# Performance work log

Measured on AMD Instinct MI355X. Metric: run time of the kernel, lower is better.

## Reference

```python
import jax, jax.numpy as jnp
import numpy as np

DIM = 1024
N_HEADS = 16
HEAD_DIM = DIM // N_HEADS  # 64
THETA = 10000.0
B, S = 4, 1024


def _rope_full_dim(x):
    """RoPE applied over the FULL last dim (head_dim == model dim), matching the
    original module which builds RotaryEmbeddings(head_dim=args.dim) and applies
    it to [B, S, dim] before splitting into heads. Positions start at 0."""
    Bx, Sx, D = x.shape
    freq = 1.0 / (THETA ** (jnp.arange(0, D, 2, dtype=jnp.float32) / D))  # [D/2]
    ang = jnp.arange(Sx, dtype=jnp.float32)[:, None] * freq[None, :]      # [S, D/2]
    cos, sin = jnp.cos(ang), jnp.sin(ang)
    xp = x.astype(jnp.float32).reshape(Bx, Sx, D // 2, 2)
    x0, x1 = xp[..., 0], xp[..., 1]
    rot = jnp.stack([x0 * cos - x1 * sin, x0 * sin + x1 * cos], axis=-1)
    return rot.reshape(Bx, Sx, D).astype(x.dtype)


def setup_inputs() -> dict:
    key = jax.random.key(0)
    ks = jax.random.split(key, 5)
    scale = 1.0 / np.sqrt(DIM)
    x = jax.random.normal(ks[0], (B, S, DIM), dtype=jnp.float32)
    Wq = jax.random.normal(ks[1], (DIM, DIM), dtype=jnp.float32) * scale
    Wk = jax.random.normal(ks[2], (DIM, DIM), dtype=jnp.float32) * scale
    Wv = jax.random.normal(ks[3], (DIM, DIM), dtype=jnp.float32) * scale
    Wo = jax.random.normal(ks[4], (DIM, DIM), dtype=jnp.float32) * scale
    bo = jnp.zeros((DIM,), dtype=jnp.float32)
    return {"x": x, "Wq": Wq, "Wk": Wk, "Wv": Wv, "Wo": Wo, "bo": bo, "start_pos": 0}


def reference(x, Wq, Wk, Wv, Wo, bo, start_pos):
    # start_pos == 0: the zero-initialized KV cache write+read is an identity
    # (keys == xk, values == xv over [:, :S]); n_rep == 1 so repeat_kv is a no-op.
    # NOTE: the original applies NO causal mask.
    Bx, Sx, _ = x.shape
    xq = _rope_full_dim(x @ Wq.T)  # [B, S, DIM] (weights stored torch-style [out,in])
    xk = _rope_full_dim(x @ Wk.T)
    xv = x @ Wv.T
    q = xq.reshape(Bx, Sx, N_HEADS, HEAD_DIM).transpose(0, 2, 1, 3)  # [B,H,S,D]
    k = xk.reshape(Bx, Sx, N_HEADS, HEAD_DIM).transpose(0, 2, 1, 3)
    v = xv.reshape(Bx, Sx, N_HEADS, HEAD_DIM).transpose(0, 2, 1, 3)
    scores = jnp.einsum("bhqd,bhkd->bhqk", q, k) / np.float32(np.sqrt(HEAD_DIM))
    attn = jax.nn.softmax(scores.astype(jnp.float32), axis=-1).astype(q.dtype)
    out = jnp.einsum("bhqk,bhkd->bhqd", attn, v)          # [B,H,S,D]
    out = out.transpose(0, 2, 1, 3).reshape(Bx, Sx, DIM)  # [B,S,DIM]
    return out @ Wo.T + bo
```

## Files before the change

### kernel.cpp

```cpp
#include <hip/hip_runtime.h>
#include <cstdint>
#include <cstddef>

typedef _Float16 f16;
typedef __attribute__((ext_vector_type(8))) _Float16 h8v;
typedef __attribute__((ext_vector_type(4))) _Float16 h4v;
typedef __attribute__((ext_vector_type(4))) float f4v;

#define DIM 1024
#define SEQ 1024
#define NH 16
#define HD 64

__device__ __forceinline__ void gld16(const void* g, void* l) {
  __builtin_amdgcn_global_load_lds(
      (const __attribute__((address_space(1))) void*)g,
      (__attribute__((address_space(3))) void*)l, 16, 0, 0);
}

__device__ __forceinline__ f4v mfma16(h8v a, h8v b, f4v c) {
  return __builtin_amdgcn_mfma_f32_16x16x32_f16(a, b, c, 0, 0, 0);
}

__device__ __forceinline__ void cvt_store4(f16* dst, float4 v) {
  *(h4v*)dst = (h4v){(f16)v.x, (f16)v.y, (f16)v.z, (f16)v.w};
}

__global__ __launch_bounds__(256) void convert_kernel(
    const float* __restrict__ x,  const float* __restrict__ Wq,
    const float* __restrict__ Wk, const float* __restrict__ Wv,
    const float* __restrict__ Wo,
    f16* __restrict__ xh, f16* __restrict__ wqkv, f16* __restrict__ woh)
{
  int i = blockIdx.x * 256 + threadIdx.x;
  cvt_store4(xh + 4 * (size_t)i, ((const float4*)x)[i]);
  if (i < DIM * DIM / 4) {
    cvt_store4(wqkv + 4 * (size_t)i,               ((const float4*)Wq)[i]);
    cvt_store4(wqkv + DIM * DIM + 4 * (size_t)i,   ((const float4*)Wk)[i]);
    cvt_store4(wqkv + 2 * DIM * DIM + 4 * (size_t)i, ((const float4*)Wv)[i]);
    cvt_store4(woh + 4 * (size_t)i,                ((const float4*)Wo)[i]);
  }
}

__global__ __launch_bounds__(256) void qkv_gemm(
    const f16* __restrict__ A, const f16* __restrict__ W,
    f16* __restrict__ Qh, f16* __restrict__ Kh, f16* __restrict__ Vt)
{
  __shared__ f16 lA[128 * 32];
  __shared__ f16 lB[128 * 32];
  const int m0 = blockIdx.x * 128;
  const int n0 = blockIdx.y * 128;
  const int tid = threadIdx.x;
  const int w = tid >> 6, lane = tid & 63, quad = lane >> 4, l16 = lane & 15;
  const int wm = (w >> 1) * 64, wn = (w & 1) * 64;

  const int c0 = tid, c1 = 256 + tid;
  const int r0 = c0 >> 2, kc0 = (c0 & 3) ^ ((r0 >> 1) & 3);
  const int r1 = c1 >> 2, kc1 = (c1 & 3) ^ ((r1 >> 1) & 3);
  const f16* gA0 = A + (size_t)(m0 + r0) * DIM + kc0 * 8;
  const f16* gA1 = A + (size_t)(m0 + r1) * DIM + kc1 * 8;
  const f16* gB0 = W + (size_t)(n0 + r0) * DIM + kc0 * 8;
  const f16* gB1 = W + (size_t)(n0 + r1) * DIM + kc1 * 8;
  f16* lA0 = &lA[(c0 & ~63) * 8];
  f16* lA1 = &lA[(c1 & ~63) * 8];
  f16* lB0 = &lB[(c0 & ~63) * 8];
  f16* lB1 = &lB[(c1 & ~63) * 8];

  int pA[4], pB[4];
#pragma unroll
  for (int t = 0; t < 4; ++t) {
    int r = wm + t * 16 + l16;
    pA[t] = r * 4 + (quad ^ ((r >> 1) & 3));
    int rn = wn + t * 16 + l16;
    pB[t] = rn * 4 + (quad ^ ((rn >> 1) & 3));
  }

  f4v acc[4][4] = {};
  for (int kt = 0; kt < DIM / 32; ++kt) {
    const int ko = kt * 32;
    gld16(gA0 + ko, lA0);
    gld16(gA1 + ko, lA1);
    gld16(gB0 + ko, lB0);
    gld16(gB1 + ko, lB1);
    __syncthreads();
    h8v af[4], bf[4];
#pragma unroll
    for (int t = 0; t < 4; ++t) af[t] = *(const h8v*)&lA[pA[t] * 8];
#pragma unroll
    for (int t = 0; t < 4; ++t) bf[t] = *(const h8v*)&lB[pB[t] * 8];
#pragma unroll
    for (int i = 0; i < 4; ++i)
#pragma unroll
      for (int j = 0; j < 4; ++j)
        acc[i][j] = mfma16(af[i], bf[j], acc[i][j]);
    __syncthreads();
  }

  if (n0 < 2 * DIM) {
    f16* dst = (n0 < DIM) ? Qh : Kh;
#pragma unroll
    for (int i = 0; i < 4; ++i) {
      const int mb = m0 + wm + i * 16 + quad * 4;
#pragma unroll
      for (int j = 0; j < 4; ++j) {
        const int n = n0 + wn + j * 16 + l16;
        const int d = n & (DIM - 1);
        const float fr = exp2f(-0.025952563f * (float)(d >> 1));
        const float sgn = (d & 1) ? 1.0f : -1.0f;
        const int hh = d >> 6, dd = d & 63;
#pragma unroll
        for (int r = 0; r < 4; ++r) {
          const int m = mb + r;
          const int s = m & (SEQ - 1), b = m >> 10;
          const float v = acc[i][j][r];
          const float pt = __shfl_xor(v, 1, 64);
          float sn, cs;
          __sincosf((float)s * fr, &sn, &cs);
          dst[((size_t)(b * NH + hh) * SEQ + s) * HD + dd] =
              (f16)(v * cs + sgn * pt * sn);
        }
      }
    }
  } else {
#pragma unroll
    for (int i = 0; i < 4; ++i) {
      const int mb = m0 + wm + i * 16 + quad * 4;
      const int s = mb & (SEQ - 1), b = mb >> 10;
#pragma unroll
      for (int j = 0; j < 4; ++j) {
        const int d = (n0 - 2 * DIM) + wn + j * 16 + l16;
        const int hh = d >> 6, dd = d & 63;
        h4v vv = {(f16)acc[i][j][0], (f16)acc[i][j][1],
                  (f16)acc[i][j][2], (f16)acc[i][j][3]};
        *(h4v*)&Vt[((size_t)(b * NH + hh) * HD + dd) * SEQ + s] = vv;
      }
    }
  }
}

__global__ __launch_bounds__(256) void attn_kernel(
    const f16* __restrict__ Q, const f16* __restrict__ K,
    const f16* __restrict__ V, f16* __restrict__ O)
{
  __shared__ f16 lK[64 * 64];
  __shared__ f16 lV[64 * 64];
  __shared__ f16 lP[4][16 * 72];
  const int tid = threadIdx.x;
  const int w = tid >> 6, lane = tid & 63, quad = lane >> 4, l16 = lane & 15;
  const int qt = blockIdx.x, bh = blockIdx.y;
  const f16* Qb = Q + (size_t)bh * SEQ * HD;
  const f16* Kb = K + (size_t)bh * SEQ * HD;
  const f16* Vb = V + (size_t)bh * HD * SEQ;
  const int q0 = qt * 64;
  const int qrow = q0 + w * 16 + l16;

  h8v aq0 = *(const h8v*)&Qb[(size_t)qrow * HD + quad * 8];
  h8v aq1 = *(const h8v*)&Qb[(size_t)qrow * HD + quad * 8 + 32];
  aq0 = aq0 * (f16)0.125f;
  aq1 = aq1 * (f16)0.125f;

  const int c0 = tid, c1 = 256 + tid;
  const int r0 = c0 >> 3, kc0 = (c0 & 7) ^ (r0 & 7);
  const int r1 = c1 >> 3, kc1 = (c1 & 7) ^ (r1 & 7);
  const f16* gK0 = Kb + (size_t)r0 * HD + kc0 * 8;
  const f16* gK1 = Kb + (size_t)r1 * HD + kc1 * 8;
  const f16* gV0 = Vb + (size_t)r0 * SEQ + kc0 * 8;
  const f16* gV1 = Vb + (size_t)r1 * SEQ + kc1 * 8;
  f16* lK0 = &lK[(c0 & ~63) * 8];
  f16* lK1 = &lK[(c1 & ~63) * 8];
  f16* lV0 = &lV[(c0 & ~63) * 8];
  f16* lV1 = &lV[(c1 & ~63) * 8];

  int pbt[4][2];
#pragma unroll
  for (int j = 0; j < 4; ++j) {
    int r = j * 16 + l16;
#pragma unroll
    for (int kk = 0; kk < 2; ++kk)
      pbt[j][kk] = r * 8 + ((quad + 4 * kk) ^ (r & 7));
  }

  float mr[4], lr[4];
  f4v accO[4] = {};
#pragma unroll
  for (int r = 0; r < 4; ++r) { mr[r] = -1e30f; lr[r] = 0.f; }

  for (int t = 0; t < SEQ / 64; ++t) {
    const int key0 = t * 64;
    __syncthreads();
    gld16(gK0 + (size_t)key0 * HD, lK0);
    gld16(gK1 + (size_t)key0 * HD, lK1);
    gld16(gV0 + key0, lV0);
    gld16(gV1 + key0, lV1);
    __syncthreads();

    f4v sc[4];
#pragma unroll
    for (int j = 0; j < 4; ++j) {
      f4v z = {};
      z = mfma16(aq0, *(const h8v*)&lK[pbt[j][0] * 8], z);
      z = mfma16(aq1, *(const h8v*)&lK[pbt[j][1] * 8], z);
      sc[j] = z;
    }
    float tmax[4];
#pragma unroll
    for (int r = 0; r < 4; ++r) {
      float tm = fmaxf(fmaxf(sc[0][r], sc[1][r]), fmaxf(sc[2][r], sc[3][r]));
#pragma unroll
      for (int off = 1; off < 16; off <<= 1)
        tm = fmaxf(tm, __shfl_xor(tm, off, 64));
      tmax[r] = tm;
    }
    float alpha[4], mnew[4];
#pragma unroll
    for (int r = 0; r < 4; ++r) {
      mnew[r] = fmaxf(mr[r], tmax[r]);
      alpha[r] = __expf(mr[r] - mnew[r]);
      mr[r] = mnew[r];
    }
    float p[4][4];
    float rs[4] = {0.f, 0.f, 0.f, 0.f};
#pragma unroll
    for (int j = 0; j < 4; ++j)
#pragma unroll
      for (int r = 0; r < 4; ++r) {
        p[j][r] = __expf(sc[j][r] - mnew[r]);
        rs[r] += p[j][r];
      }
#pragma unroll
    for (int r = 0; r < 4; ++r) {
#pragma unroll
      for (int off = 1; off < 16; off <<= 1)
        rs[r] += __shfl_xor(rs[r], off, 64);
      lr[r] = lr[r] * alpha[r] + rs[r];
    }
    f4v av = {alpha[0], alpha[1], alpha[2], alpha[3]};
#pragma unroll
    for (int j = 0; j < 4; ++j) accO[j] *= av;

    f16* Pw = lP[w];
#pragma unroll
    for (int j = 0; j < 4; ++j)
#pragma unroll
      for (int r = 0; r < 4; ++r)
        Pw[(quad * 4 + r) * 72 + j * 16 + l16] = (f16)p[j][r];
    h8v pa0 = *(const h8v*)&Pw[l16 * 72 + quad * 8];
    h8v pa1 = *(const h8v*)&Pw[l16 * 72 + quad * 8 + 32];
#pragma unroll
    for (int j = 0; j < 4; ++j) {
      accO[j] = mfma16(pa0, *(const h8v*)&lV[pbt[j][0] * 8], accO[j]);
      accO[j] = mfma16(pa1, *(const h8v*)&lV[pbt[j][1] * 8], accO[j]);
    }
  }

  const int b = bh >> 4, hh = bh & 15;
  f4v inv = {1.f / lr[0], 1.f / lr[1], 1.f / lr[2], 1.f / lr[3]};
#pragma unroll
  for (int j = 0; j < 4; ++j) {
    f4v o = accO[j] * inv;
    const int d = j * 16 + l16;
#pragma unroll
    for (int r = 0; r < 4; ++r) {
      const int s = q0 + w * 16 + quad * 4 + r;
      O[(size_t)(b * SEQ + s) * DIM + hh * HD + d] = (f16)o[r];
    }
  }
}

__global__ __launch_bounds__(256) void out_gemm(
    const f16* __restrict__ A, const f16* __restrict__ W,
    const float* __restrict__ bias, float* __restrict__ out)
{
  __shared__ f16 lA[64 * 32];
  __shared__ f16 lB[128 * 32];
  const int m0 = blockIdx.x * 64;
  const int n0 = blockIdx.y * 128;
  const int tid = threadIdx.x;
  const int w = tid >> 6, lane = tid & 63, quad = lane >> 4, l16 = lane & 15;
  const int wm = (w >> 1) * 32, wn = (w & 1) * 64;

  const int c0 = tid, c1 = 256 + tid;
  const int rA = c0 >> 2, kcA = (c0 & 3) ^ ((rA >> 1) & 3);
  const int rB1 = c1 >> 2, kcB1 = (c1 & 3) ^ ((rB1 >> 1) & 3);
  const f16* gA  = A + (size_t)(m0 + rA) * DIM + kcA * 8;
  const f16* gB0 = W + (size_t)(n0 + rA) * DIM + kcA * 8;
  const f16* gB1 = W + (size_t)(n0 + rB1) * DIM + kcB1 * 8;
  f16* lAp  = &lA[(c0 & ~63) * 8];
  f16* lB0p = &lB[(c0 & ~63) * 8];
  f16* lB1p = &lB[(c1 & ~63) * 8];

  int pA_[2], pB_[4];
#pragma unroll
  for (int t = 0; t < 2; ++t) {
    int r = wm + t * 16 + l16;
    pA_[t] = r * 4 + (quad ^ ((r >> 1) & 3));
  }
#pragma unroll
  for (int t = 0; t < 4; ++t) {
    int rn = wn + t * 16 + l16;
    pB_[t] = rn * 4 + (quad ^ ((rn >> 1) & 3));
  }

  f4v acc[2][4] = {};
  for (int kt = 0; kt < DIM / 32; ++kt) {
    const int ko = kt * 32;
    gld16(gA + ko, lAp);
    gld16(gB0 + ko, lB0p);
    gld16(gB1 + ko, lB1p);
    __syncthreads();
    h8v af[2], bf[4];
#pragma unroll
    for (int t = 0; t < 2; ++t) af[t] = *(const h8v*)&lA[pA_[t] * 8];
#pragma unroll
    for (int t = 0; t < 4; ++t) bf[t] = *(const h8v*)&lB[pB_[t] * 8];
#pragma unroll
    for (int i = 0; i < 2; ++i)
#pragma unroll
      for (int j = 0; j < 4; ++j)
        acc[i][j] = mfma16(af[i], bf[j], acc[i][j]);
    __syncthreads();
  }

#pragma unroll
  for (int i = 0; i < 2; ++i) {
#pragma unroll
    for (int j = 0; j < 4; ++j) {
      const int n = n0 + wn + j * 16 + l16;
      const float bv = bias[n];
#pragma unroll
      for (int r = 0; r < 4; ++r) {
        const int m = m0 + wm + i * 16 + quad * 4 + r;
        out[(size_t)m * DIM + n] = acc[i][j][r] + bv;
      }
    }
  }
}

extern "C" void kernel_launch(void* const* d_in, const int* in_sizes, int n_in,
                              void* d_out, int out_size, void* d_ws, size_t ws_size,
                              hipStream_t stream)
{
  (void)in_sizes; (void)n_in; (void)out_size; (void)ws_size;
  const float* x  = (const float*)d_in[0];
  const float* Wq = (const float*)d_in[1];
  const float* Wk = (const float*)d_in[2];
  const float* Wv = (const float*)d_in[3];
  const float* Wo = (const float*)d_in[4];
  const float* bo = (const float*)d_in[5];
  float* out = (float*)d_out;

  char* ws = (char*)d_ws;
  const size_t MB = (size_t)1 << 20;
  f16* xh   = (f16*)(ws);
  f16* wqkv = (f16*)(ws + 8  * MB);
  f16* woh  = (f16*)(ws + 14 * MB);
  f16* Qh   = (f16*)(ws + 16 * MB);
  f16* Kh   = (f16*)(ws + 24 * MB);
  f16* Vt   = (f16*)(ws + 32 * MB);
  f16* Oh   = (f16*)(ws);

  convert_kernel<<<dim3(4096), 256, 0, stream>>>(x, Wq, Wk, Wv, Wo, xh, wqkv, woh);
  qkv_gemm<<<dim3(32, 24), 256, 0, stream>>>(xh, wqkv, Qh, Kh, Vt);
  attn_kernel<<<dim3(16, 64), 256, 0, stream>>>(Qh, Kh, Vt, Oh);
  out_gemm<<<dim3(64, 8), 256, 0, stream>>>(Oh, woh, bo, out);
}
```

Measured before the change: 194.8 us.

## Compute transposed S^T in attention to keep P in registers, drop LDS staging

The QK^T MFMA now takes K as the A operand and Q as B, so each lane holds scores for a single query column across keys. That makes the row max and row sum reductions two cross-quad shuffles instead of four-step butterflies per row. The score accumulator layout then serves directly as the A operand of 16x16x16 MFMAs for P*V, which removes the per-wave LDS write/read round trip for P. In exchange, alpha and the final 1/l must be redistributed with shuffles, and P*V uses twice as many smaller-K MFMAs with new V-tile addressing.

```diff
diff --git a/kernel.cpp b/kernel.cpp
--- a/kernel.cpp
+++ b/kernel.cpp
@@ -20,6 +20,9 @@
 
 __device__ __forceinline__ f4v mfma16(h8v a, h8v b, f4v c) {
   return __builtin_amdgcn_mfma_f32_16x16x32_f16(a, b, c, 0, 0, 0);
+}
+__device__ __forceinline__ f4v mfma16k16(h4v a, h4v b, f4v c) {
+  return __builtin_amdgcn_mfma_f32_16x16x16f16(a, b, c, 0, 0, 0);
 }
 
 __device__ __forceinline__ void cvt_store4(f16* dst, float4 v) {
@@ -144,7 +147,6 @@
 {
   __shared__ f16 lK[64 * 64];
   __shared__ f16 lV[64 * 64];
-  __shared__ f16 lP[4][16 * 72];
   const int tid = threadIdx.x;
   const int w = tid >> 6, lane = tid & 63, quad = lane >> 4, l16 = lane & 15;
   const int qt = blockIdx.x, bh = blockIdx.y;
@@ -154,10 +156,10 @@
   const int q0 = qt * 64;
   const int qrow = q0 + w * 16 + l16;
 
-  h8v aq0 = *(const h8v*)&Qb[(size_t)qrow * HD + quad * 8];
-  h8v aq1 = *(const h8v*)&Qb[(size_t)qrow * HD + quad * 8 + 32];
-  aq0 = aq0 * (f16)0.125f;
-  aq1 = aq1 * (f16)0.125f;
+  h8v bq0 = *(const h8v*)&Qb[(size_t)qrow * HD + quad * 8];
+  h8v bq1 = *(const h8v*)&Qb[(size_t)qrow * HD + quad * 8 + 32];
+  bq0 = bq0 * (f16)0.125f;
+  bq1 = bq1 * (f16)0.125f;
 
   const int c0 = tid, c1 = 256 + tid;
   const int r0 = c0 >> 3, kc0 = (c0 & 7) ^ (r0 & 7);
@@ -179,11 +181,15 @@
     for (int kk = 0; kk < 2; ++kk)
       pbt[j][kk] = r * 8 + ((quad + 4 * kk) ^ (r & 7));
   }
-
-  float mr[4], lr[4];
+  const f16* vbase[4];
+#pragma unroll
+  for (int j = 0; j < 4; ++j) {
+    int slot = (j * 2 + (quad >> 1)) ^ (l16 & 7);
+    vbase[j] = &lV[l16 * 64 + slot * 8 + (quad & 1) * 4];
+  }
+
+  float mr = -1e30f, lr = 0.f;
   f4v accO[4] = {};
-#pragma unroll
-  for (int r = 0; r < 4; ++r) { mr[r] = -1e30f; lr[r] = 0.f; }
 
   for (int t = 0; t < SEQ / 64; ++t) {
     const int key0 = t * 64;
@@ -198,71 +204,66 @@
 #pragma unroll
     for (int j = 0; j < 4; ++j) {
       f4v z = {};
-      z = mfma16(aq0, *(const h8v*)&lK[pbt[j][0] * 8], z);
-      z = mfma16(aq1, *(const h8v*)&lK[pbt[j][1] * 8], z);
+      z = mfma16(*(const h8v*)&lK[pbt[j][0] * 8], bq0, z);
+      z = mfma16(*(const h8v*)&lK[pbt[j][1] * 8], bq1, z);
       sc[j] = z;
     }
-    float tmax[4];
-#pragma unroll
-    for (int r = 0; r < 4; ++r) {
-      float tm = fmaxf(fmaxf(sc[0][r], sc[1][r]), fmaxf(sc[2][r], sc[3][r]));
-#pragma unroll
-      for (int off = 1; off < 16; off <<= 1)
-        tm = fmaxf(tm, __shfl_xor(tm, off, 64));
-      tmax[r] = tm;
-    }
-    float alpha[4], mnew[4];
-#pragma unroll
-    for (int r = 0; r < 4; ++r) {
-      mnew[r] = fmaxf(mr[r], tmax[r]);
-      alpha[r] = __expf(mr[r] - mnew[r]);
-      mr[r] = mnew[r];
-    }
+
+    float tm = sc[0][0];
+#pragma unroll
+    for (int j = 0; j < 4; ++j)
+#pragma unroll
+      for (int r = 0; r < 4; ++r) tm = fmaxf(tm, sc[j][r]);
+    tm = fmaxf(tm, __shfl_xor(tm, 16, 64));
+    tm = fmaxf(tm, __shfl_xor(tm, 32, 64));
+    const float mnew = fmaxf(mr, tm);
+    const float alpha = __expf(mr - mnew);
+    mr = mnew;
+
     float p[4][4];
-    float rs[4] = {0.f, 0.f, 0.f, 0.f};
+    float rs = 0.f;
 #pragma unroll
     for (int j = 0; j < 4; ++j)
 #pragma unroll
       for (int r = 0; r < 4; ++r) {
-        p[j][r] = __expf(sc[j][r] - mnew[r]);
-        rs[r] += p[j][r];
+        p[j][r] = __expf(sc[j][r] - mnew);
+        rs += p[j][r];
       }
-#pragma unroll
-    for (int r = 0; r < 4; ++r) {
-#pragma unroll
-      for (int off = 1; off < 16; off <<= 1)
-        rs[r] += __shfl_xor(rs[r], off, 64);
-      lr[r] = lr[r] * alpha[r] + rs[r];
-    }
-    f4v av = {alpha[0], alpha[1], alpha[2], alpha[3]};
-#pragma unroll
-    for (int j = 0; j < 4; ++j) accO[j] *= av;
-
-    f16* Pw = lP[w];
+    rs += __shfl_xor(rs, 16, 64);
+    rs += __shfl_xor(rs, 32, 64);
+    lr = lr * alpha + rs;
+
+    f4v av;
+#pragma unroll
+    for (int r = 0; r < 4; ++r) av[r] = __shfl(alpha, quad * 4 + r, 64);
+#pragma unroll
+    for (int dt = 0; dt < 4; ++dt) accO[dt] *= av;
+
+    h4v pf[4];
 #pragma unroll
     for (int j = 0; j < 4; ++j)
-#pragma unroll
-      for (int r = 0; r < 4; ++r)
-        Pw[(quad * 4 + r) * 72 + j * 16 + l16] = (f16)p[j][r];
-    h8v pa0 = *(const h8v*)&Pw[l16 * 72 + quad * 8];
-    h8v pa1 = *(const h8v*)&Pw[l16 * 72 + quad * 8 + 32];
-#pragma unroll
-    for (int j = 0; j < 4; ++j) {
-      accO[j] = mfma16(pa0, *(const h8v*)&lV[pbt[j][0] * 8], accO[j]);
-      accO[j] = mfma16(pa1, *(const h8v*)&lV[pbt[j][1] * 8], accO[j]);
-    }
-  }
+      pf[j] = (h4v){(f16)p[j][0], (f16)p[j][1], (f16)p[j][2], (f16)p[j][3]};
+
+#pragma unroll
+    for (int dt = 0; dt < 4; ++dt)
+#pragma unroll
+      for (int j = 0; j < 4; ++j)
+        accO[dt] = mfma16k16(pf[j], *(const h4v*)(vbase[j] + dt * 1024),
+                             accO[dt]);
+  }
+
+  f4v invl;
+#pragma unroll
+  for (int r = 0; r < 4; ++r) invl[r] = 1.0f / __shfl(lr, quad * 4 + r, 64);
 
   const int b = bh >> 4, hh = bh & 15;
-  f4v inv = {1.f / lr[0], 1.f / lr[1], 1.f / lr[2], 1.f / lr[3]};
-#pragma unroll
-  for (int j = 0; j < 4; ++j) {
-    f4v o = accO[j] * inv;
-    const int d = j * 16 + l16;
+#pragma unroll
+  for (int dt = 0; dt < 4; ++dt) {
+    const int d = dt * 16 + l16;
 #pragma unroll
     for (int r = 0; r < 4; ++r) {
       const int s = q0 + w * 16 + quad * 4 + r;
-      O[(size_t)(b * SEQ + s) * DIM + hh * HD + d] = (f16)o[r];
+      O[(size_t)(b * SEQ + s) * DIM + hh * HD + d] = (f16)(accO[dt][r] * invl[r]);
     }
   }
 }
```

Measured after the change: 181.0 us. 1.08x faster.
